# Optimization experiments

Hardware: AMD Instinct MI355X
Metric: run time of the kernel (lower is better)

The kernel has to match this reference:

```python
import jax, jax.numpy as jnp
import numpy as np

L, B, T, D, V = 4, 32, 512, 512, 1000


def setup_inputs() -> dict:
    key = jax.random.key(0)
    k0, k1, k2, k3, k4 = jax.random.split(key, 5)
    ids = jax.random.randint(k0, (B, T), 0, V)
    mask = jax.random.randint(k1, (B, T), 0, 2).astype(bool)  # True = valid token
    emb = jax.random.normal(k2, (V, D), dtype=jnp.float32) * 0.1
    W = jax.random.normal(k3, (L, D, 3 * D), dtype=jnp.float32) / np.float32(np.sqrt(D))
    v = jax.random.normal(k4, (L, 2, D), dtype=jnp.float32) * 0.1  # (v_f, v_r) per layer
    b = jnp.zeros((L, 2, D), dtype=jnp.float32)                    # (b_f, b_r) per layer
    return {"ids": ids, "mask": mask, "emb": emb, "W": W, "v": v, "b": b}


def _sru_layer(x, pad, Wl, vf, vr, bf, br):
    # x: [T,B,D] layer input; pad: [T,B,1] bool (True = padded step)
    Tn, Bn, Dn = x.shape
    U = jnp.einsum('tbd,de->tbe', x, Wl).reshape(Tn, Bn, 3, Dn)
    xt, fpre, rpre = U[:, :, 0], U[:, :, 1], U[:, :, 2]

    def step(c, inp):
        xt_t, fp_t, rp_t, x_t, pad_t = inp
        f = jax.nn.sigmoid(fp_t + vf * c + bf)
        r = jax.nn.sigmoid(rp_t + vr * c + br)
        c_new = f * c + (1.0 - f) * xt_t
        h = r * jnp.tanh(c_new) + (1.0 - r) * x_t  # highway (input_size==hidden_size)
        c_out = jnp.where(pad_t, c, c_new)          # padded step: keep state
        h = jnp.where(pad_t, 0.0, h)                # padded step: zero output
        return c_out, h

    c0 = jnp.zeros_like(x[0])  # zero initial hidden state, as in the torch code
    _, h = jax.lax.scan(step, c0, (xt, fpre, rpre, x, pad))
    return h  # [T,B,D]


def reference(ids, mask, emb, W, v, b):
    x = emb[ids]                       # CharEmbedder lookup: [B,T,D]
    x = jnp.transpose(x, (1, 0, 2))    # [T,B,D]  (permute(1,0,2))
    pad = (~mask).T[:, :, None]        # inverted_mask.T -> [T,B,1]
    for l in range(L):
        x = _sru_layer(x, pad, W[l], v[l, 0], v[l, 1], b[l, 0], b[l, 1])
    return jnp.transpose(x, (1, 0, 2))  # back to [B,T,D]
```

## Files before the change

kernel.cpp:

```cpp
#include <hip/hip_runtime.h>
#include <hip/hip_bf16.h>


#define LAYERS 4
#define BB 32
#define TT 512
#define DD 512
#define N3 1536
#define MROWS (TT * BB)
#define WPL ((size_t)DD * N3)
#define SB 32
#define LOG2E 1.4426950408889634f
#define TWOLOG2E 2.8853900817779268f

typedef unsigned short u16;
typedef unsigned int u32;
typedef _Float16 half8 __attribute__((ext_vector_type(8)));
typedef float f32x4 __attribute__((ext_vector_type(4)));

#define SBAR() asm volatile("s_barrier" ::: "memory")
#define WAITVM(n) asm volatile("s_waitcnt vmcnt(" n ")" ::: "memory")

__device__ __forceinline__ float b2f(u16 u) {
  union { unsigned int i; float f; } x;
  x.i = ((unsigned int)u) << 16;
  return x.f;
}
__device__ __forceinline__ u16 f2h(float f) {
  _Float16 h = (_Float16)f;
  return *(u16*)&h;
}
__device__ __forceinline__ float h2f(u16 u) {
  _Float16 h;
  *(u16*)&h = u;
  return (float)h;
}
__device__ __forceinline__ float rcpf(float x) { return __builtin_amdgcn_rcpf(x); }
__device__ __forceinline__ float exp2f_(float x) { return __builtin_amdgcn_exp2f(x); }

__device__ __forceinline__ void async_ld16(const void* g, void* l) {
  __builtin_amdgcn_global_load_lds(
      (const __attribute__((address_space(1))) void*)g,
      (__attribute__((address_space(3))) void*)l, 16, 0, 0);
}
__device__ __forceinline__ void async_ld4(const void* g, void* l) {
  __builtin_amdgcn_global_load_lds(
      (const __attribute__((address_space(1))) void*)g,
      (__attribute__((address_space(3))) void*)l, 4, 0, 0);
}

__global__ void detect_kernel(const u16* __restrict__ emb_u,
                              const int* __restrict__ mask_i,
                              const int* __restrict__ ids_i,
                              int* __restrict__ flags) {
  __shared__ int cnt[3];
  __shared__ int zc;
  int tid = threadIdx.x;
  if (tid < 3) cnt[tid] = 0;
  if (tid == 0) zc = 0;
  __syncthreads();
  int bad = 0, zero_even = 0;
  for (int i = tid; i < 8192; i += 256) {
    u16 u = emb_u[i];
    unsigned e = (u >> 7) & 0xFF;
    if (e >= 0x8F) bad++;
    if ((i & 1) == 0 && u == 0) zero_even++;
  }
  if (bad) atomicAdd(&cnt[0], bad);
  if (zero_even) atomicAdd(&zc, zero_even);
  if (tid < 64) {
    unsigned vv = (unsigned)mask_i[tid];
    if (vv > 1u) atomicAdd(&cnt[1], 1);
  }
  if (tid < 256) {
    if (ids_i[2 * tid + 1] == 0) atomicAdd(&cnt[2], 1);
  }
  __syncthreads();
  if (tid == 0) {
    flags[0] = (cnt[0] > 64 || zc > 3000) ? 1 : 0;
    flags[1] = (cnt[1] > 0) ? 1 : 0;
    flags[2] = (cnt[2] >= 192) ? 1 : 0;
  }
}

__global__ __launch_bounds__(256)
void wprep_kernel(const void* __restrict__ W, u16* __restrict__ W16,
                  const int* __restrict__ flags) {
  __shared__ float tileW[32][33];
  int l = blockIdx.z;
  int k0 = blockIdx.x * 32;
  int n0 = blockIdx.y * 32;
  int tx = threadIdx.x & 31;
  int ty = threadIdx.x >> 5;
  int ff = flags[0];
  const float* Wf = (const float*)W + (size_t)l * WPL;
  const u16* Wb = (const u16*)W + (size_t)l * WPL;
  for (int kk = ty; kk < 32; kk += 8) {
    size_t off = (size_t)(k0 + kk) * N3 + n0 + tx;
    tileW[kk][tx] = ff ? Wf[off] : b2f(Wb[off]);
  }
  __syncthreads();
  u16* outP = W16 + (size_t)l * WPL;
  for (int nn = ty; nn < 32; nn += 8) {
    float x = tileW[tx][nn];
    outP[(size_t)(n0 + nn) * DD + k0 + tx] = f2h(x);
  }
}

__global__ void embed_kernel(const int* __restrict__ ids,
                             const void* __restrict__ emb,
                             u16* __restrict__ X16,
                             const int* __restrict__ flags) {
  int i = blockIdx.x * 256 + threadIdx.x;
  int d = i & (DD - 1);
  int tb = i >> 9;
  int b = tb & (BB - 1);
  int t = tb >> 5;
  int ii = b * TT + t;
  int id = flags[2] ? ids[2 * ii] : ids[ii];
  float val = flags[0] ? ((const float*)emb)[id * DD + d]
                       : b2f(((const u16*)emb)[id * DD + d]);
  X16[i] = f2h(val);
}

__global__ __launch_bounds__(512, 2)
void gemm_kernel(const u16* __restrict__ X16, const u16* __restrict__ W16l,
                 const void* __restrict__ bvec, int layer,
                 const int* __restrict__ flags,
                 u16* __restrict__ U16, int row_base, int chunkM, int nblk) {
  __shared__ u16 ldsA[2][2][8192];
  __shared__ u16 ldsB[2][2][4096];
  const int tid = threadIdx.x;
  const int lane = tid & 63, wave = tid >> 6;
  const int wm = wave >> 1, wn = wave & 1;
  const int m16 = lane & 15, quad = lane >> 4;

  const int orig = blockIdx.x;
  const int wg = (orig & 7) * (nblk >> 3) + (orig >> 3);
  const int mt = wg / 12, nt = wg - mt * 12;

  const int arow0 = row_base + mt * 256;
  const int bcol0 = nt * 128;

  const int srow = lane >> 2;
  const int sq = (lane & 3) ^ ((lane >> 3) & 3);
  const u16* pa = X16 + (size_t)(arow0 + wave * 32 + srow) * DD + sq * 8;
  const u16* pb = W16l + (size_t)(bcol0 + wave * 16 + srow) * DD + sq * 8;

  auto stage = [&](int h) {
    const int ts = h >> 1, kk = h & 1, db = ts & 1;
    const int kv = ts * 64 + kk * 32;
    async_ld16(pa + kv, &ldsA[db][kk][(2 * wave) * 512]);
    async_ld16(pa + kv + (size_t)16 * DD, &ldsA[db][kk][(2 * wave + 1) * 512]);
    async_ld16(pb + kv, &ldsB[db][kk][wave * 512]);
  };

  f32x4 acc[4][4];
#pragma unroll
  for (int mi = 0; mi < 4; ++mi)
#pragma unroll
    for (int ni = 0; ni < 4; ++ni)
#pragma unroll
      for (int r = 0; r < 4; ++r) acc[mi][ni][r] = 0.f;

  stage(0); stage(1); stage(2);
  WAITVM("6");
  SBAR();

  const int loff = m16 * 32 + (quad ^ ((m16 >> 1) & 3)) * 8;

#pragma unroll
  for (int t = 0; t < 8; ++t) {
    const int db = t & 1;
#pragma unroll
    for (int kk = 0; kk < 2; ++kk) {
      const int g = 2 * t + kk;
      half8 af[4], bf[4];
#pragma unroll
      for (int i = 0; i < 4; ++i)
        af[i] = *(const half8*)&ldsA[db][kk][(wm * 4 + i) * 512 + loff];
#pragma unroll
      for (int i = 0; i < 4; ++i)
        bf[i] = *(const half8*)&ldsB[db][kk][(wn * 4 + i) * 512 + loff];
      if (g + 3 < 16) stage(g + 3);
      __builtin_amdgcn_s_setprio(1);
#pragma unroll
      for (int mi = 0; mi < 4; ++mi)
#pragma unroll
        for (int ni = 0; ni < 4; ++ni)
          acc[mi][ni] = __builtin_amdgcn_mfma_f32_16x16x32_f16(
              af[mi], bf[ni], acc[mi][ni], 0, 0, 0);
      __builtin_amdgcn_s_setprio(0);
      if (g <= 12) WAITVM("6");
      else if (g == 13) WAITVM("3");
      else if (g == 14) WAITVM("0");
      SBAR();
    }
  }

  const int ff = flags[0];
  const int pl = nt >> 2;
  const int dd0 = (nt & 3) * 128;
  u16* up = U16 + (size_t)pl * chunkM * 512;
  const int r0 = mt * 256 + wm * 64 + quad * 4;
  const int c0 = dd0 + wn * 64 + m16;
  if (pl == 0) {
#pragma unroll
    for (int mi = 0; mi < 4; ++mi)
#pragma unroll
      for (int reg = 0; reg < 4; ++reg) {
        size_t rb = (size_t)(r0 + mi * 16 + reg) * 512 + c0;
#pragma unroll
        for (int ni = 0; ni < 4; ++ni)
          up[rb + ni * 16] = f2h(acc[mi][ni][reg]);
      }
  } else {
    float bias[4];
#pragma unroll
    for (int ni = 0; ni < 4; ++ni) {
      size_t bo = (size_t)layer * 2 * DD + (size_t)(pl - 1) * DD + c0 + ni * 16;
      bias[ni] = ff ? ((const float*)bvec)[bo] : b2f(((const u16*)bvec)[bo]);
    }
#pragma unroll
    for (int mi = 0; mi < 4; ++mi)
#pragma unroll
      for (int reg = 0; reg < 4; ++reg) {
        size_t rb = (size_t)(r0 + mi * 16 + reg) * 512 + c0;
#pragma unroll
        for (int ni = 0; ni < 4; ++ni)
          up[rb + ni * 16] = f2h(-(acc[mi][ni][reg] + bias[ni]) * LOG2E);
      }
  }
}

template <int EMIT>
__global__ __launch_bounds__(448, 1)
void scan_kernel(const u16* __restrict__ U16, float* __restrict__ X,
                 u16* __restrict__ X16,
                 const void* __restrict__ mask_p, const void* __restrict__ vbase,
                 int layer, const int* __restrict__ flags,
                 float* __restrict__ carry, int t0, int nt, int chunkM) {
  __shared__ u16 bufA[2][2][SB][64];
  __shared__ u16 bufB[3][2][SB][64];
  __shared__ float ring[2][2][SB][64];
  __shared__ int msk[TT];
  const int tid = threadIdx.x;
  const int wave = tid >> 6, lane = tid & 63;
  const int idx0 = blockIdx.x * 64;
  const int b = idx0 >> 9;
  const int d0 = idx0 & 511;
  const int ff = flags[0], fm = flags[1];

  const int* mi_ = (const int*)mask_p + b * TT;
  const unsigned char* mb_ = (const unsigned char*)mask_p + b * TT;
  for (int i = tid; i < nt; i += 448) msk[i] = fm ? (int)mb_[t0 + i] : mi_[t0 + i];

  float vfs = 0.f, vrs = 0.f, c = 0.f;
  {
    int d = d0 + lane;
    size_t voff = (size_t)layer * 2 * DD;
    if (wave == 0) {
      float vf = ff ? ((const float*)vbase)[voff + d]
                    : b2f(((const u16*)vbase)[voff + d]);
      vfs = -vf * LOG2E;
      c = (t0 == 0) ? 0.f : carry[idx0 + lane];
    } else if (wave >= 1 && wave <= 4) {
      float vr = ff ? ((const float*)vbase)[voff + DD + d]
                    : b2f(((const u16*)vbase)[voff + DD + d]);
      vrs = -vr * LOG2E;
    }
  }

  const int nbuf = nt / SB;

  auto ld_pair = [&](const u16* rowS, const u16* rowS1, void* ldst) {
    const u32* a0 = (const u32*)rowS;
    const u32* a1 = (const u32*)rowS1;
    const u32* ga = (lane < 32) ? (a0 + lane) : (a1 + (lane - 32));
    async_ld4(ga, ldst);
  };

  auto produceA = [&](int k) {
    int ph = k & 1, tl = k * SB;
    const u16* p0 = U16 + ((size_t)tl * BB + b) * 512 + d0;
    const u16* p1 = p0 + (size_t)chunkM * 512;
#pragma unroll
    for (int s = 0; s < SB; s += 2)
      ld_pair(p0 + (size_t)s * BB * 512, p0 + (size_t)(s + 1) * BB * 512,
              &bufA[ph][0][s][0]);
#pragma unroll
    for (int s = 0; s < SB; s += 2)
      ld_pair(p1 + (size_t)s * BB * 512, p1 + (size_t)(s + 1) * BB * 512,
              &bufA[ph][1][s][0]);
  };
  auto produceB = [&](int k) {
    int ph = k % 3, tl = k * SB;
    const u16* p2 = U16 + 2 * (size_t)chunkM * 512 + ((size_t)tl * BB + b) * 512 + d0;
    const u16* xb = X16 + ((size_t)(t0 + tl) * BB + b) * DD + d0;
#pragma unroll
    for (int s = 0; s < SB; s += 2)
      ld_pair(p2 + (size_t)s * BB * 512, p2 + (size_t)(s + 1) * BB * 512,
              &bufB[ph][0][s][0]);
#pragma unroll
    for (int s = 0; s < SB; s += 2)
      ld_pair(xb + (size_t)s * BB * DD, xb + (size_t)(s + 1) * BB * DD,
              &bufB[ph][1][s][0]);
  };

  float* Xp = X + (size_t)b * TT * DD + d0 + lane;

  auto hphase = [&](int j, int hw) {
    int phc = j & 1, phb = j % 3;
    int sbase = hw * (SB / 4);
#pragma unroll
    for (int si = 0; si < SB / 4; ++si) {
      int s = sbase + si;
      float cprev = ring[phc][0][s][lane];
      float cn = ring[phc][1][s][lane];
      float rps = h2f(bufB[phb][0][s][lane]);
      float xin = h2f(bufB[phb][1][s][lane]);
      int m = msk[j * SB + s];
      float tr = exp2f_(fmaf(vrs, cprev, rps));
      float r = rcpf(1.f + tr);
      float e2 = exp2f_(cn * TWOLOG2E);
      float th = fmaf(-2.f, rcpf(e2 + 1.f), 1.f);
      float h = fmaf(r, th - xin, xin);
      float hout = (m == 0) ? 0.f : h;
      int tg = t0 + j * SB + s;
      if (EMIT)
        X16[((size_t)tg * BB + b) * DD + d0 + lane] = f2h(hout);
      else
        Xp[(size_t)tg * DD] = hout;
    }
  };

  if (wave == 5) produceA(0);
  if (wave == 6) produceB(0);

  for (int k = 0; k < nbuf; ++k) {
    __syncthreads();
    if (wave == 5) {
      if (k + 1 < nbuf) produceA(k + 1);
    } else if (wave == 6) {
      if (k + 1 < nbuf) produceB(k + 1);
    } else if (wave == 0) {
      int ph = k & 1;
#pragma unroll 8
      for (int s = 0; s < SB; ++s) {
        float xt = h2f(bufA[ph][0][s][lane]);
        float fps = h2f(bufA[ph][1][s][lane]);
        float t = exp2f_(fmaf(vfs, c, fps));
        float f = rcpf(1.f + t);
        float cn = fmaf(f, c - xt, xt);
        ring[ph][0][s][lane] = c;
        ring[ph][1][s][lane] = cn;
        c = (msk[k * SB + s] == 0) ? c : cn;
      }
    } else {
      if (k > 0) hphase(k - 1, wave - 1);
    }
  }
  __syncthreads();
  if (wave >= 1 && wave <= 4) hphase(nbuf - 1, wave - 1);
  if (wave == 0) carry[idx0 + lane] = c;
}

__global__ void sentinel_kernel(float* out) { out[threadIdx.x] = 12345.f; }

extern "C" void kernel_launch(void* const* d_in, const int* in_sizes, int n_in,
                              void* d_out, int out_size, void* d_ws, size_t ws_size,
                              hipStream_t stream) {
  const int* ids = (const int*)d_in[0];
  const void* mask = d_in[1];
  const void* emb = d_in[2];
  const void* W = d_in[3];
  const void* v = d_in[4];
  const void* bp = d_in[5];

  char* ws = (char*)d_ws;
  int* flags = (int*)ws;
  float* carry = (float*)(ws + 4096);
  const size_t offX16 = 69632;
  const size_t offW16 = offX16 + (size_t)MROWS * DD * 2;
  const size_t offU = offW16 + (size_t)LAYERS * WPL * 2;
  const size_t perT = (size_t)BB * N3 * 2;

  const int cand[4] = {512, 256, 128, 64};
  int chunkT = 0;
  for (int i = 0; i < 4; ++i) {
    if (ws_size >= offU + (size_t)cand[i] * perT) { chunkT = cand[i]; break; }
  }
  if (!chunkT) {
    sentinel_kernel<<<1, 256, 0, stream>>>((float*)d_out);
    return;
  }
  const int chunkM = chunkT * BB;

  u16* X16 = (u16*)(ws + offX16);
  u16* W16 = (u16*)(ws + offW16);
  u16* U16 = (u16*)(ws + offU);
  float* X = (float*)d_out;

  detect_kernel<<<1, 256, 0, stream>>>((const u16*)emb, (const int*)mask,
                                       (const int*)ids, flags);
  wprep_kernel<<<dim3(16, 48, 4), 256, 0, stream>>>(W, W16, flags);
  embed_kernel<<<MROWS * DD / 256, 256, 0, stream>>>(ids, emb, X16, flags);

  int nch = TT / chunkT;
  for (int l = 0; l < LAYERS; ++l) {
    const u16* W16l = W16 + (size_t)l * WPL;
    for (int ch = 0; ch < nch; ++ch) {
      int t0 = ch * chunkT;
      int nblk = (chunkM / 256) * 12;
      gemm_kernel<<<nblk, 512, 0, stream>>>(X16, W16l, bp, l, flags, U16,
                                            t0 * BB, chunkM, nblk);
      if (l < LAYERS - 1)
        scan_kernel<1><<<BB * DD / 64, 448, 0, stream>>>(U16, X, X16, mask, v, l,
                                                         flags, carry, t0, chunkT,
                                                         chunkM);
      else
        scan_kernel<0><<<BB * DD / 64, 448, 0, stream>>>(U16, X, X16, mask, v, l,
                                                         flags, carry, t0, chunkT,
                                                         chunkM);
    }
  }
}
```

Baseline: 368.4 us.

## Use 4-wave GEMM blocks with 128x64 warp tiles and triple-buffered LDS

Halves the GEMM block size to 256 threads so each wave computes a 128x64 output tile (8x4 MFMA accumulators) instead of 64x64. The K loop now uses a 3-slot LDS ring with one 32-wide K step per iteration, replacing the 2x2 double buffer, and prefetches two steps ahead. The goal is more register-level reuse of B fragments and fewer barriers per MFMA. The cost is doubled accumulator register pressure, which may spill or lower occupancy, and the wait counts must match the new load counts per stage.

```diff
diff --git a/kernel.cpp b/kernel.cpp
--- a/kernel.cpp
+++ b/kernel.cpp
@@ -123,13 +123,13 @@
   X16[i] = f2h(val);
 }
 
-__global__ __launch_bounds__(512, 2)
+__global__ __launch_bounds__(256, 2)
 void gemm_kernel(const u16* __restrict__ X16, const u16* __restrict__ W16l,
                  const void* __restrict__ bvec, int layer,
                  const int* __restrict__ flags,
                  u16* __restrict__ U16, int row_base, int chunkM, int nblk) {
-  __shared__ u16 ldsA[2][2][8192];
-  __shared__ u16 ldsB[2][2][4096];
+  __shared__ u16 ldsA[3][8192];
+  __shared__ u16 ldsB[3][4096];
   const int tid = threadIdx.x;
   const int lane = tid & 63, wave = tid >> 6;
   const int wm = wave >> 1, wn = wave & 1;
@@ -144,69 +144,71 @@
 
   const int srow = lane >> 2;
   const int sq = (lane & 3) ^ ((lane >> 3) & 3);
-  const u16* pa = X16 + (size_t)(arow0 + wave * 32 + srow) * DD + sq * 8;
-  const u16* pb = W16l + (size_t)(bcol0 + wave * 16 + srow) * DD + sq * 8;
-
-  auto stage = [&](int h) {
-    const int ts = h >> 1, kk = h & 1, db = ts & 1;
-    const int kv = ts * 64 + kk * 32;
-    async_ld16(pa + kv, &ldsA[db][kk][(2 * wave) * 512]);
-    async_ld16(pa + kv + (size_t)16 * DD, &ldsA[db][kk][(2 * wave + 1) * 512]);
-    async_ld16(pb + kv, &ldsB[db][kk][wave * 512]);
+  const u16* pa = X16 + (size_t)(arow0 + wave * 64 + srow) * DD + sq * 8;
+  const u16* pb = W16l + (size_t)(bcol0 + wave * 32 + srow) * DD + sq * 8;
+
+  auto stage = [&](int t) {
+    const int sl = t % 3;
+    const int kv = t * 32;
+    u16* da = &ldsA[sl][(wave * 4) * 512];
+    const u16* sa = pa + kv;
+#pragma unroll
+    for (int j = 0; j < 4; ++j)
+      async_ld16(sa + (size_t)16 * j * DD, da + j * 512);
+    u16* db_ = &ldsB[sl][(wave * 2) * 512];
+    const u16* sb = pb + kv;
+#pragma unroll
+    for (int j = 0; j < 2; ++j)
+      async_ld16(sb + (size_t)16 * j * DD, db_ + j * 512);
   };
 
-  f32x4 acc[4][4];
-#pragma unroll
-  for (int mi = 0; mi < 4; ++mi)
+  f32x4 acc[8][4];
+#pragma unroll
+  for (int mi = 0; mi < 8; ++mi)
 #pragma unroll
     for (int ni = 0; ni < 4; ++ni)
 #pragma unroll
       for (int r = 0; r < 4; ++r) acc[mi][ni][r] = 0.f;
 
-  stage(0); stage(1); stage(2);
+  stage(0); stage(1);
   WAITVM("6");
   SBAR();
 
   const int loff = m16 * 32 + (quad ^ ((m16 >> 1) & 3)) * 8;
 
 #pragma unroll
-  for (int t = 0; t < 8; ++t) {
-    const int db = t & 1;
-#pragma unroll
-    for (int kk = 0; kk < 2; ++kk) {
-      const int g = 2 * t + kk;
-      half8 af[4], bf[4];
-#pragma unroll
-      for (int i = 0; i < 4; ++i)
-        af[i] = *(const half8*)&ldsA[db][kk][(wm * 4 + i) * 512 + loff];
-#pragma unroll
-      for (int i = 0; i < 4; ++i)
-        bf[i] = *(const half8*)&ldsB[db][kk][(wn * 4 + i) * 512 + loff];
-      if (g + 3 < 16) stage(g + 3);
-      __builtin_amdgcn_s_setprio(1);
-#pragma unroll
-      for (int mi = 0; mi < 4; ++mi)
-#pragma unroll
-        for (int ni = 0; ni < 4; ++ni)
-          acc[mi][ni] = __builtin_amdgcn_mfma_f32_16x16x32_f16(
-              af[mi], bf[ni], acc[mi][ni], 0, 0, 0);
-      __builtin_amdgcn_s_setprio(0);
-      if (g <= 12) WAITVM("6");
-      else if (g == 13) WAITVM("3");
-      else if (g == 14) WAITVM("0");
-      SBAR();
-    }
+  for (int t = 0; t < 16; ++t) {
+    const int sl = t % 3;
+    half8 af[8], bf[4];
+#pragma unroll
+    for (int i = 0; i < 8; ++i)
+      af[i] = *(const half8*)&ldsA[sl][(wm * 8 + i) * 512 + loff];
+#pragma unroll
+    for (int i = 0; i < 4; ++i)
+      bf[i] = *(const half8*)&ldsB[sl][(wn * 4 + i) * 512 + loff];
+    if (t + 2 < 16) stage(t + 2);
+    __builtin_amdgcn_s_setprio(1);
+#pragma unroll
+    for (int mi = 0; mi < 8; ++mi)
+#pragma unroll
+      for (int ni = 0; ni < 4; ++ni)
+        acc[mi][ni] = __builtin_amdgcn_mfma_f32_16x16x32_f16(
+            af[mi], bf[ni], acc[mi][ni], 0, 0, 0);
+    __builtin_amdgcn_s_setprio(0);
+    if (t <= 13) WAITVM("6");
+    else if (t == 14) WAITVM("0");
+    if (t < 15) SBAR();
   }
 
   const int ff = flags[0];
   const int pl = nt >> 2;
   const int dd0 = (nt & 3) * 128;
   u16* up = U16 + (size_t)pl * chunkM * 512;
-  const int r0 = mt * 256 + wm * 64 + quad * 4;
+  const int r0 = mt * 256 + wm * 128 + quad * 4;
   const int c0 = dd0 + wn * 64 + m16;
   if (pl == 0) {
 #pragma unroll
-    for (int mi = 0; mi < 4; ++mi)
+    for (int mi = 0; mi < 8; ++mi)
 #pragma unroll
       for (int reg = 0; reg < 4; ++reg) {
         size_t rb = (size_t)(r0 + mi * 16 + reg) * 512 + c0;
@@ -222,7 +224,7 @@
       bias[ni] = ff ? ((const float*)bvec)[bo] : b2f(((const u16*)bvec)[bo]);
     }
 #pragma unroll
-    for (int mi = 0; mi < 4; ++mi)
+    for (int mi = 0; mi < 8; ++mi)
 #pragma unroll
       for (int reg = 0; reg < 4; ++reg) {
         size_t rb = (size_t)(r0 + mi * 16 + reg) * 512 + c0;
@@ -412,7 +414,7 @@
     for (int ch = 0; ch < nch; ++ch) {
       int t0 = ch * chunkT;
       int nblk = (chunkM / 256) * 12;
-      gemm_kernel<<<nblk, 512, 0, stream>>>(X16, W16l, bp, l, flags, U16,
+      gemm_kernel<<<nblk, 256, 0, stream>>>(X16, W16l, bp, l, flags, U16,
                                             t0 * BB, chunkM, nblk);
       if (l < LAYERS - 1)
         scan_kernel<1><<<BB * DD / 64, 448, 0, stream>>>(U16, X, X16, mask, v, l,
```

New measurement: 348.4 us. 5.4% less time.

## Use a 4-slot LDS ring and double-buffer GEMM fragments in registers

Applied to the files above, without the earlier changes.

The projection GEMM's LDS staging changes from a double buffer with two k-halves to a 4-slot ring indexed by the k-step. Fragments for the next step are loaded from LDS into a second register set while the MFMAs for the current step run, so LDS read latency is hidden behind matrix math. The vmcnt waits are retuned, and the final barrier is dropped. Launch bounds drop to one block per CU to leave room for the extra registers, which may reduce occupancy.

```diff
diff --git a/kernel.cpp b/kernel.cpp
--- a/kernel.cpp
+++ b/kernel.cpp
@@ -123,13 +123,13 @@
   X16[i] = f2h(val);
 }
 
-__global__ __launch_bounds__(512, 2)
+__global__ __launch_bounds__(512, 1)
 void gemm_kernel(const u16* __restrict__ X16, const u16* __restrict__ W16l,
                  const void* __restrict__ bvec, int layer,
                  const int* __restrict__ flags,
                  u16* __restrict__ U16, int row_base, int chunkM, int nblk) {
-  __shared__ u16 ldsA[2][2][8192];
-  __shared__ u16 ldsB[2][2][4096];
+  __shared__ u16 ldsA[4][8192];
+  __shared__ u16 ldsB[4][4096];
   const int tid = threadIdx.x;
   const int lane = tid & 63, wave = tid >> 6;
   const int wm = wave >> 1, wn = wave & 1;
@@ -147,12 +147,12 @@
   const u16* pa = X16 + (size_t)(arow0 + wave * 32 + srow) * DD + sq * 8;
   const u16* pb = W16l + (size_t)(bcol0 + wave * 16 + srow) * DD + sq * 8;
 
-  auto stage = [&](int h) {
-    const int ts = h >> 1, kk = h & 1, db = ts & 1;
-    const int kv = ts * 64 + kk * 32;
-    async_ld16(pa + kv, &ldsA[db][kk][(2 * wave) * 512]);
-    async_ld16(pa + kv + (size_t)16 * DD, &ldsA[db][kk][(2 * wave + 1) * 512]);
-    async_ld16(pb + kv, &ldsB[db][kk][wave * 512]);
+  auto stage = [&](int t) {
+    const int sl = t & 3;
+    const int kv = t * 32;
+    async_ld16(pa + kv, &ldsA[sl][(2 * wave) * 512]);
+    async_ld16(pa + kv + (size_t)16 * DD, &ldsA[sl][(2 * wave + 1) * 512]);
+    async_ld16(pb + kv, &ldsB[sl][wave * 512]);
   };
 
   f32x4 acc[4][4];
@@ -164,38 +164,41 @@
       for (int r = 0; r < 4; ++r) acc[mi][ni][r] = 0.f;
 
   stage(0); stage(1); stage(2);
-  WAITVM("6");
+  WAITVM("3");
   SBAR();
 
   const int loff = m16 * 32 + (quad ^ ((m16 >> 1) & 3)) * 8;
 
-#pragma unroll
-  for (int t = 0; t < 8; ++t) {
-    const int db = t & 1;
-#pragma unroll
-    for (int kk = 0; kk < 2; ++kk) {
-      const int g = 2 * t + kk;
-      half8 af[4], bf[4];
-#pragma unroll
-      for (int i = 0; i < 4; ++i)
-        af[i] = *(const half8*)&ldsA[db][kk][(wm * 4 + i) * 512 + loff];
-#pragma unroll
-      for (int i = 0; i < 4; ++i)
-        bf[i] = *(const half8*)&ldsB[db][kk][(wn * 4 + i) * 512 + loff];
-      if (g + 3 < 16) stage(g + 3);
-      __builtin_amdgcn_s_setprio(1);
-#pragma unroll
-      for (int mi = 0; mi < 4; ++mi)
-#pragma unroll
-        for (int ni = 0; ni < 4; ++ni)
-          acc[mi][ni] = __builtin_amdgcn_mfma_f32_16x16x32_f16(
-              af[mi], bf[ni], acc[mi][ni], 0, 0, 0);
-      __builtin_amdgcn_s_setprio(0);
-      if (g <= 12) WAITVM("6");
-      else if (g == 13) WAITVM("3");
-      else if (g == 14) WAITVM("0");
-      SBAR();
-    }
+  half8 af[2][4], bf[2][4];
+#pragma unroll
+  for (int i = 0; i < 4; ++i) {
+    af[0][i] = *(const half8*)&ldsA[0][(wm * 4 + i) * 512 + loff];
+    bf[0][i] = *(const half8*)&ldsB[0][(wn * 4 + i) * 512 + loff];
+  }
+
+#pragma unroll
+  for (int t = 0; t < 16; ++t) {
+    const int cur = t & 1, nxt = cur ^ 1;
+    if (t + 3 < 16) stage(t + 3);
+    if (t + 1 < 16) {
+      const int sl1 = (t + 1) & 3;
+#pragma unroll
+      for (int i = 0; i < 4; ++i) {
+        af[nxt][i] = *(const half8*)&ldsA[sl1][(wm * 4 + i) * 512 + loff];
+        bf[nxt][i] = *(const half8*)&ldsB[sl1][(wn * 4 + i) * 512 + loff];
+      }
+    }
+    __builtin_amdgcn_s_setprio(1);
+#pragma unroll
+    for (int mi = 0; mi < 4; ++mi)
+#pragma unroll
+      for (int ni = 0; ni < 4; ++ni)
+        acc[mi][ni] = __builtin_amdgcn_mfma_f32_16x16x32_f16(
+            af[cur][mi], bf[cur][ni], acc[mi][ni], 0, 0, 0);
+    __builtin_amdgcn_s_setprio(0);
+    if (t <= 12) WAITVM("3");
+    else if (t == 13) WAITVM("0");
+    if (t <= 13) SBAR();
   }
 
   const int ff = flags[0];
```

Measured after the change: 364.2 us. Within noise of the previous version (-1.2%).
